# Optimization experiments

Measured on AMD Instinct MI355X. Metric: run time of the kernel, lower is better.

The kernel has to match this reference:

```python
import jax, jax.numpy as jnp
import numpy as np

SIGMA = 10.0
EPSILON = 46.0
BATCH = 4096
D_X = 1024
D_Y = 512


def setup_inputs() -> dict:
    key = jax.random.key(0)
    kx, ky = jax.random.split(key)
    x = jax.random.normal(kx, (BATCH, D_X), dtype=jnp.float32)
    y = jax.random.normal(ky, (BATCH, D_Y), dtype=jnp.float32)
    return {"x": x, "y": y}


def _pairwise_l2(a):
    # [B, B] matrix of ||a_i - a_j||_2 via the matmul trick; safe sqrt for grads.
    sq = jnp.sum(a * a, axis=-1)                      # [B]
    d2 = sq[:, None] + sq[None, :] - 2.0 * (a @ a.T)  # [B, B]
    d2 = jnp.maximum(d2, 0.0)
    return jnp.sqrt(jnp.where(d2 > 1e-12, d2, 1e-12))


def reference(x, y):
    b = x.shape[0]
    dx = _pairwise_l2(x)   # ||x_i - x_j||
    dy = _pairwise_l2(y)   # ||y_i - y_j||
    offdiag = 1.0 - jnp.eye(b, dtype=x.dtype)          # i != j
    mask = offdiag * (dx <= EPSILON).astype(x.dtype)   # threshold at epsilon
    w = jnp.exp(-dx / SIGMA)                           # heat-kernel weight
    loss = jnp.sum(mask * w * dy)
    return loss
```

## Files before the change

### kernel.cpp

```cpp
#include <hip/hip_runtime.h>
#include <hip/hip_bf16.h>
#include <hip/hip_fp8.h>
#include <stdint.h>

#define BATCH 4096
#define D_X   1024
#define D_Y   512

constexpr float SIGMA_INV = 0.1f;
constexpr float EPS_THR   = 46.0f;

constexpr int BMF   = 128;
constexpr int NTF   = BATCH / BMF;
constexpr int NBLKF = NTF * (NTF + 1) / 2;
constexpr int XS8   = D_X / 16;
constexpr int YS8   = D_Y / 16;

constexpr int BM = 128;
constexpr int NT = BATCH / BM;
constexpr int NBLK = NT * (NT + 1) / 2;

typedef __bf16 bf16x8 __attribute__((ext_vector_type(8)));
typedef float  f32x4  __attribute__((ext_vector_type(4)));
typedef unsigned short u16x8 __attribute__((ext_vector_type(8)));
typedef unsigned long long u64;
typedef u64 u64x2 __attribute__((ext_vector_type(2)));

__device__ __forceinline__ unsigned short f32_to_bf16_bits(float f) {
    unsigned int u = __builtin_bit_cast(unsigned int, f);
    unsigned int r = (u + 0x7FFFu + ((u >> 16) & 1u)) >> 16;
    return (unsigned short)r;
}

__device__ __forceinline__ int perm16(int u8) {
    int ks = u8 >> 2, kg = u8 & 3;
    return (ks >> 1) * 8 + kg * 2 + (ks & 1);
}

__global__ void __launch_bounds__(192)
convert_fp8(const float* __restrict__ x, const float* __restrict__ y,
            u64* __restrict__ xq, u64* __restrict__ yq,
            float* __restrict__ sqx, float* __restrict__ sqy) {
    __shared__ float part[2];
    const int row = blockIdx.x;
    const int t   = threadIdx.x;
    const int lane = t & 63;
    const int wid  = t >> 6;

    float nrm = 0.f;
    if (t < 128) {
        const float4* p = (const float4*)(x + (size_t)row * D_X + t * 8);
        float4 f0 = p[0], f1 = p[1];
        float e[8] = {f0.x, f0.y, f0.z, f0.w, f1.x, f1.y, f1.z, f1.w};
        u64 w = 0;
#pragma unroll
        for (int i = 0; i < 8; ++i) {
            __hip_fp8_e4m3 q(e[i]);
            float b = (float)q;
            nrm = fmaf(b, b, nrm);
            w |= (u64)q.__x << (8 * i);
        }
        xq[(size_t)row * 128 + (t & ~15) + perm16(t & 15)] = w;
    } else {
        int o = t - 128;
        const float4* p = (const float4*)(y + (size_t)row * D_Y + o * 8);
        float4 f0 = p[0], f1 = p[1];
        float e[8] = {f0.x, f0.y, f0.z, f0.w, f1.x, f1.y, f1.z, f1.w};
        u64 w = 0;
#pragma unroll
        for (int i = 0; i < 8; ++i) {
            __hip_fp8_e4m3 q(e[i]);
            float b = (float)q;
            nrm = fmaf(b, b, nrm);
            w |= (u64)q.__x << (8 * i);
        }
        yq[(size_t)row * 64 + (o & ~15) + perm16(o & 15)] = w;
    }
#pragma unroll
    for (int off = 32; off > 0; off >>= 1)
        nrm += __shfl_down(nrm, off, 64);
    if (lane == 0) {
        if (wid < 2) part[wid] = nrm;
        else         sqy[row] = nrm;
    }
    __syncthreads();
    if (t == 0) sqx[row] = part[0] + part[1];
}


__device__ __forceinline__ u64x2 ldsfrag2(const u16x8* T, int row, int c) {
    int slot = c ^ (row & 7);
    return __builtin_bit_cast(u64x2, T[row * 8 + slot]);
}

#define ISSUE(DST, BASE, OFF)                                              \
    {                                                                      \
        _Pragma("unroll")                                                  \
        for (int it = 0; it < 8; ++it)                                     \
            __builtin_amdgcn_global_load_lds(                              \
                (const uint32_t __attribute__((address_space(1)))*)(BASE[it] + (OFF)), \
                (uint32_t __attribute__((address_space(3)))*)((DST) + it * 256 + wid * 64), \
                16, 0, 0);                                                 \
    }

#define FRAGS_READ(BUF)                                                    \
        u64x2 fa[2][4], fb[2][4];                      \
        _Pragma("unroll")                                                  \
        for (int t2 = 0; t2 < 2; ++t2) {                                   \
            _Pragma("unroll")                                              \
            for (int m = 0; m < 4; ++m)                                    \
                fa[t2][m] = ldsfrag2(BUF, wr * 64 + m * 16 + lrow,         \
                                     t2 * 4 + kgrp);                       \
            _Pragma("unroll")                                              \
            for (int n = 0; n < 4; ++n)                                    \
                fb[t2][n] = ldsfrag2(BUF, 128 + wc * 64 + n * 16 + lrow,   \
                                     t2 * 4 + kgrp);                       \
        }

#define FRAGS_MFMA(ACC)                                                    \
        __builtin_amdgcn_s_setprio(1);                                     \
        _Pragma("unroll")                                                  \
        for (int t2 = 0; t2 < 2; ++t2)                                     \
            _Pragma("unroll")                                              \
            for (int h = 0; h < 2; ++h)                                    \
                _Pragma("unroll")                                          \
                for (int m = 0; m < 4; ++m)                                \
                    _Pragma("unroll")                                      \
                    for (int n = 0; n < 4; ++n)                            \
                        ACC[m][n] =                                        \
                            __builtin_amdgcn_mfma_f32_16x16x32_fp8_fp8(    \
                                (long)fa[t2][m][h], (long)fb[t2][n][h],    \
                                ACC[m][n], 0, 0, 0);                       \
        __builtin_amdgcn_s_setprio(0);

#define GSTEP(BUF, ACC, W, IBASE, IOFF)                                    \
    {                                                                      \
        asm volatile("s_waitcnt vmcnt(" #W ")" ::: "memory");              \
        __builtin_amdgcn_s_barrier();                                      \
        FRAGS_READ(BUF)                                                    \
        asm volatile("s_waitcnt lgkmcnt(0)" ::: "memory");                 \
        __builtin_amdgcn_s_barrier();                                      \
        ISSUE(BUF, IBASE, IOFF)                                            \
        FRAGS_MFMA(ACC)                                                    \
    }
#define GSTEP_NOISSUE(BUF, ACC, W)                                         \
    {                                                                      \
        asm volatile("s_waitcnt vmcnt(" #W ")" ::: "memory");              \
        __builtin_amdgcn_s_barrier();                                      \
        FRAGS_READ(BUF)                                                    \
        FRAGS_MFMA(ACC)                                                    \
    }

__global__ void __launch_bounds__(256, 2)
gram_fp8(const u16x8* __restrict__ xq, const u16x8* __restrict__ yq,
         const float* __restrict__ sqx, const float* __restrict__ sqy,
         float* __restrict__ out) {
    __shared__ u16x8 T0[2048], T1[2048];
    __shared__ float snxA[BMF], snxB[BMF], snyA[BMF], snyB[BMF];
    __shared__ float wsum[4];

    const int tid  = threadIdx.x;
    const int lane = tid & 63;
    const int wid  = tid >> 6;
    const int wr   = wid >> 1;
    const int wc   = wid & 1;
    const int lrow = lane & 15;
    const int kgrp = lane >> 4;

    int sb = (blockIdx.x & 7) * (NBLKF / 8) + (blockIdx.x >> 3);

    int t0 = sb, bi = 0;
    while (t0 >= NTF - bi) { t0 -= NTF - bi; ++bi; }
    const int bj = bi + t0;
    const int iA = bi * BMF;
    const int iB = bj * BMF;
    const bool diag = (bi == bj);

    if (tid < BMF) {
        snxA[tid] = sqx[iA + tid];
        snyA[tid] = sqy[iA + tid];
    } else {
        int u = tid - BMF;
        snxB[u] = sqx[iB + u];
        snyB[u] = sqy[iB + u];
    }

    const char* g[8];
#pragma unroll
    for (int it = 0; it < 8; ++it) {
        int ul   = it * 256 + wid * 64 + lane;
        int row  = ul >> 3;
        int st   = ul & 7;
        int lg   = st ^ (row & 7);
        int grow = (row < 128 ? iA + row : iB + row - 128);
        g[it] = (const char*)xq + (size_t)grow * (XS8 * 16) + lg * 16;
    }

    f32x4 accX[4][4] = {};
    f32x4 accY[4][4] = {};

    ISSUE(T0, g, 0)
    ISSUE(T1, g, 128)

    GSTEP(T0, accX, 8, g, 256)
    GSTEP(T1, accX, 8, g, 384)
    GSTEP(T0, accX, 8, g, 512)
    GSTEP(T1, accX, 8, g, 640)
    GSTEP(T0, accX, 8, g, 768)
    GSTEP(T1, accX, 8, g, 896)

#pragma unroll
    for (int it = 0; it < 8; ++it) {
        int ul   = it * 256 + wid * 64 + lane;
        int row  = ul >> 3;
        int st   = ul & 7;
        int lg   = st ^ (row & 7);
        int grow = (row < 128 ? iA + row : iB + row - 128);
        g[it] = (const char*)yq + (size_t)grow * (YS8 * 16) + lg * 16;
    }

    GSTEP(T0, accX, 8, g, 0)
    GSTEP(T1, accX, 8, g, 128)
    GSTEP(T0, accY, 8, g, 256)
    GSTEP(T1, accY, 8, g, 384)
    GSTEP_NOISSUE(T0, accY, 8)
    GSTEP_NOISSUE(T1, accY, 0)

    float local = 0.f;
#pragma unroll
    for (int m = 0; m < 4; ++m) {
#pragma unroll
        for (int n = 0; n < 4; ++n) {
            int col   = wc * 64 + n * 16 + lrow;
            float sxj = snxB[col];
            float syj = snyB[col];
#pragma unroll
            for (int r = 0; r < 4; ++r) {
                int rowi  = wr * 64 + m * 16 + kgrp * 4 + r;
                float d2x = snxA[rowi] + sxj - 2.f * accX[m][n][r];
                float dxv = sqrtf(fmaxf(d2x, 1e-12f));
                float d2y = snyA[rowi] + syj - 2.f * accY[m][n][r];
                float dyv = sqrtf(fmaxf(d2y, 1e-12f));
                int gi = iA + rowi, gj = iB + col;
                bool keep = (gi != gj) && (dxv <= EPS_THR);
                float contrib = __expf(-dxv * SIGMA_INV) * dyv;
                local += keep ? contrib : 0.f;
            }
        }
    }
    if (!diag) local *= 2.f;

#pragma unroll
    for (int off = 32; off > 0; off >>= 1)
        local += __shfl_down(local, off, 64);
    if (lane == 0) wsum[wid] = local;
    __syncthreads();
    if (tid == 0)
        atomicAdd(out, wsum[0] + wsum[1] + wsum[2] + wsum[3]);
}

__global__ void norms_kernel_fb(const float* __restrict__ x,
                                const float* __restrict__ y,
                                float* __restrict__ sqx,
                                float* __restrict__ sqy) {
    int row = blockIdx.x;
    int t   = threadIdx.x;
    const float4* xr = (const float4*)(x + (size_t)row * D_X);
    float sx = 0.f;
#pragma unroll
    for (int i = 0; i < D_X / 4 / 64; ++i) {
        float4 v = xr[t + i * 64];
        sx += v.x * v.x + v.y * v.y + v.z * v.z + v.w * v.w;
    }
    const float4* yr = (const float4*)(y + (size_t)row * D_Y);
    float sy = 0.f;
#pragma unroll
    for (int i = 0; i < D_Y / 4 / 64; ++i) {
        float4 v = yr[t + i * 64];
        sy += v.x * v.x + v.y * v.y + v.z * v.z + v.w * v.w;
    }
#pragma unroll
    for (int off = 32; off > 0; off >>= 1) {
        sx += __shfl_down(sx, off, 64);
        sy += __shfl_down(sy, off, 64);
    }
    if (t == 0) { sqx[row] = sx; sqy[row] = sy; }
}

__device__ __forceinline__ void stage_tile_fb(const float* __restrict__ src, int ld,
                                              int base_row, int k0,
                                              u16x8* __restrict__ dst, int tid) {
#pragma unroll
    for (int it = 0; it < 2; ++it) {
        int u   = tid + it * 256;
        int row = u >> 2;
        int q   = u & 3;
        const float4* p = (const float4*)(src + (size_t)(base_row + row) * ld + k0 + q * 16);
        float4 f0 = p[0], f1 = p[1], f2 = p[2], f3 = p[3];
        u16x8 lo, hi;
        lo[0] = f32_to_bf16_bits(f0.x); lo[1] = f32_to_bf16_bits(f0.y);
        lo[2] = f32_to_bf16_bits(f0.z); lo[3] = f32_to_bf16_bits(f0.w);
        lo[4] = f32_to_bf16_bits(f1.x); lo[5] = f32_to_bf16_bits(f1.y);
        lo[6] = f32_to_bf16_bits(f1.z); lo[7] = f32_to_bf16_bits(f1.w);
        hi[0] = f32_to_bf16_bits(f2.x); hi[1] = f32_to_bf16_bits(f2.y);
        hi[2] = f32_to_bf16_bits(f2.z); hi[3] = f32_to_bf16_bits(f2.w);
        hi[4] = f32_to_bf16_bits(f3.x); hi[5] = f32_to_bf16_bits(f3.y);
        hi[6] = f32_to_bf16_bits(f3.z); hi[7] = f32_to_bf16_bits(f3.w);
        int swz = row & 7;
        dst[row * 8 + ((2 * q) ^ swz)]     = lo;
        dst[row * 8 + ((2 * q + 1) ^ swz)] = hi;
    }
}

__device__ __forceinline__ void mfma16_fb(const bf16x8 a[4], const bf16x8 b[4],
                                          f32x4 acc[4][4]) {
#pragma unroll
    for (int m = 0; m < 4; ++m)
#pragma unroll
        for (int n = 0; n < 4; ++n)
            acc[m][n] = __builtin_amdgcn_mfma_f32_16x16x32_bf16(
                a[m], b[n], acc[m][n], 0, 0, 0);
}

__device__ __forceinline__ void load_frags_fb(const u16x8* As_, const u16x8* Bs_,
                                              int wr, int wc, int lrow, int kgrp,
                                              bf16x8 a[2][4], bf16x8 b[2][4]) {
#pragma unroll
    for (int ks = 0; ks < 2; ++ks) {
#pragma unroll
        for (int m = 0; m < 4; ++m) {
            int row  = wr * 64 + m * 16 + lrow;
            int slot = (ks * 4 + kgrp) ^ (row & 7);
            a[ks][m] = __builtin_bit_cast(bf16x8, As_[row * 8 + slot]);
        }
#pragma unroll
        for (int n = 0; n < 4; ++n) {
            int row  = wc * 64 + n * 16 + lrow;
            int slot = (ks * 4 + kgrp) ^ (row & 7);
            b[ks][n] = __builtin_bit_cast(bf16x8, Bs_[row * 8 + slot]);
        }
    }
}

__global__ void __launch_bounds__(256, 2)
graph_loss_fb(const float* __restrict__ x, const float* __restrict__ y,
              const float* __restrict__ sqx, const float* __restrict__ sqy,
              float* __restrict__ out) {
    __shared__ u16x8 As[BM * 8];
    __shared__ u16x8 Bs[BM * 8];
    __shared__ float snxA[BM], snxB[BM], snyA[BM], snyB[BM];
    __shared__ float wsum[4];

    const int tid  = threadIdx.x;
    const int lane = tid & 63;
    const int wid  = tid >> 6;
    const int wr   = wid >> 1;
    const int wc   = wid & 1;
    const int lrow = lane & 15;
    const int kgrp = lane >> 4;

    int t = blockIdx.x, bi = 0;
    while (t >= NT - bi) { t -= NT - bi; ++bi; }
    const int bj = bi + t;
    const int iA = bi * BM;
    const int iB = bj * BM;

    if (tid < BM) {
        snxA[tid] = sqx[iA + tid];
        snyA[tid] = sqy[iA + tid];
        snxB[tid] = sqx[iB + tid];
        snyB[tid] = sqy[iB + tid];
    }

    f32x4 accX[4][4] = {};
    f32x4 accY[4][4] = {};
    bf16x8 a[2][4], b[2][4];

    for (int kt = 0; kt < D_X / 64; ++kt) {
        __syncthreads();
        stage_tile_fb(x, D_X, iA, kt * 64, As, tid);
        stage_tile_fb(x, D_X, iB, kt * 64, Bs, tid);
        __syncthreads();
        load_frags_fb(As, Bs, wr, wc, lrow, kgrp, a, b);
#pragma unroll
        for (int ks = 0; ks < 2; ++ks) mfma16_fb(a[ks], b[ks], accX);
    }
    for (int kt = 0; kt < D_Y / 64; ++kt) {
        __syncthreads();
        stage_tile_fb(y, D_Y, iA, kt * 64, As, tid);
        stage_tile_fb(y, D_Y, iB, kt * 64, Bs, tid);
        __syncthreads();
        load_frags_fb(As, Bs, wr, wc, lrow, kgrp, a, b);
#pragma unroll
        for (int ks = 0; ks < 2; ++ks) mfma16_fb(a[ks], b[ks], accY);
    }

    float local = 0.f;
#pragma unroll
    for (int m = 0; m < 4; ++m) {
#pragma unroll
        for (int n = 0; n < 4; ++n) {
            int col   = wc * 64 + n * 16 + lrow;
            float sxj = snxB[col];
            float syj = snyB[col];
#pragma unroll
            for (int r = 0; r < 4; ++r) {
                int rowi  = wr * 64 + m * 16 + kgrp * 4 + r;
                float d2x = snxA[rowi] + sxj - 2.f * accX[m][n][r];
                float dxv = sqrtf(fmaxf(d2x, 1e-12f));
                float d2y = snyA[rowi] + syj - 2.f * accY[m][n][r];
                float dyv = sqrtf(fmaxf(d2y, 1e-12f));
                int gi = iA + rowi, gj = iB + col;
                bool keep = (gi != gj) && (dxv <= EPS_THR);
                float contrib = __expf(-dxv * SIGMA_INV) * dyv;
                local += keep ? contrib : 0.f;
            }
        }
    }
    if (bi != bj) local *= 2.f;

#pragma unroll
    for (int off = 32; off > 0; off >>= 1)
        local += __shfl_down(local, off, 64);
    if (lane == 0) wsum[wid] = local;
    __syncthreads();
    if (tid == 0)
        atomicAdd(out, wsum[0] + wsum[1] + wsum[2] + wsum[3]);
}

extern "C" void kernel_launch(void* const* d_in, const int* in_sizes, int n_in,
                              void* d_out, int out_size, void* d_ws, size_t ws_size,
                              hipStream_t stream) {
    const float* x = (const float*)d_in[0];
    const float* y = (const float*)d_in[1];
    float* out = (float*)d_out;

    hipMemsetAsync(d_out, 0, sizeof(float) * (size_t)out_size, stream);

    const size_t xq_bytes = (size_t)BATCH * D_X;
    const size_t yq_bytes = (size_t)BATCH * D_Y;
    const size_t sq_bytes = 2 * (size_t)BATCH * sizeof(float);
    const size_t need = xq_bytes + yq_bytes + sq_bytes;

    if (ws_size >= need) {
        u64*   xq  = (u64*)d_ws;
        u64*   yq  = (u64*)((char*)d_ws + xq_bytes);
        float* sqx = (float*)((char*)d_ws + xq_bytes + yq_bytes);
        float* sqy = sqx + BATCH;
        convert_fp8<<<BATCH, 192, 0, stream>>>(x, y, xq, yq, sqx, sqy);
        gram_fp8<<<NBLKF, 256, 0, stream>>>((const u16x8*)xq, (const u16x8*)yq,
                                            sqx, sqy, out);
    } else {
        float* sqx = (float*)d_ws;
        float* sqy = sqx + BATCH;
        norms_kernel_fb<<<BATCH, 64, 0, stream>>>(x, y, sqx, sqy);
        graph_loss_fb<<<NBLK, 256, 0, stream>>>(x, y, sqx, sqy, out);
    }
}
```

Baseline: 57.33 us.

## Halve fp8 gram K-step to 64 bytes, raise occupancy to four blocks per CU

Shrinks each pipelined K-tile from 128 to 64 fp8 bytes per row, halving the LDS double buffers, and raises the launch bound to 4 blocks per SM. The fp8 packing permutation, the LDS layout (pairs of rows share a 128-byte line instead of using an XOR swizzle) and the fragment reads are reworked to match. The aim is more resident waves to hide load latency and fewer fragment registers. The cost is twice as many barrier-synchronised steps and possible LDS bank conflicts without the swizzle.

Result: slower. 59.52 us (+3.8%).

```diff
diff --git a/kernel.cpp b/kernel.cpp
--- a/kernel.cpp
+++ b/kernel.cpp
@@ -13,8 +13,8 @@
 constexpr int BMF   = 128;
 constexpr int NTF   = BATCH / BMF;
 constexpr int NBLKF = NTF * (NTF + 1) / 2;
-constexpr int XS8   = D_X / 16;
-constexpr int YS8   = D_Y / 16;
+constexpr int XRB   = D_X;
+constexpr int YRB   = D_Y;
 
 constexpr int BM = 128;
 constexpr int NT = BATCH / BM;
@@ -32,9 +32,8 @@
     return (unsigned short)r;
 }
 
-__device__ __forceinline__ int perm16(int u8) {
-    int ks = u8 >> 2, kg = u8 & 3;
-    return (ks >> 1) * 8 + kg * 2 + (ks & 1);
+__device__ __forceinline__ int perm8(int ug) {
+    return (ug & 3) * 2 + ((ug >> 2) & 1);
 }
 
 __global__ void __launch_bounds__(192)
@@ -60,7 +59,7 @@
             nrm = fmaf(b, b, nrm);
             w |= (u64)q.__x << (8 * i);
         }
-        xq[(size_t)row * 128 + (t & ~15) + perm16(t & 15)] = w;
+        xq[(size_t)row * 128 + (t & ~7) + perm8(t & 7)] = w;
     } else {
         int o = t - 128;
         const float4* p = (const float4*)(y + (size_t)row * D_Y + o * 8);
@@ -74,7 +73,7 @@
             nrm = fmaf(b, b, nrm);
             w |= (u64)q.__x << (8 * i);
         }
-        yq[(size_t)row * 64 + (o & ~15) + perm16(o & 15)] = w;
+        yq[(size_t)row * 64 + (o & ~7) + perm8(o & 7)] = w;
     }
 #pragma unroll
     for (int off = 32; off > 0; off >>= 1)
@@ -88,15 +87,10 @@
 }
 
 
-__device__ __forceinline__ u64x2 ldsfrag2(const u16x8* T, int row, int c) {
-    int slot = c ^ (row & 7);
-    return __builtin_bit_cast(u64x2, T[row * 8 + slot]);
-}
-
 #define ISSUE(DST, BASE, OFF)                                              \
     {                                                                      \
         _Pragma("unroll")                                                  \
-        for (int it = 0; it < 8; ++it)                                     \
+        for (int it = 0; it < 4; ++it)                                     \
             __builtin_amdgcn_global_load_lds(                              \
                 (const uint32_t __attribute__((address_space(1)))*)(BASE[it] + (OFF)), \
                 (uint32_t __attribute__((address_space(3)))*)((DST) + it * 256 + wid * 64), \
@@ -104,33 +98,30 @@
     }
 
 #define FRAGS_READ(BUF)                                                    \
-        u64x2 fa[2][4], fb[2][4];                      \
+        u64x2 fa[4], fb[4];                                                \
         _Pragma("unroll")                                                  \
-        for (int t2 = 0; t2 < 2; ++t2) {                                   \
-            _Pragma("unroll")                                              \
-            for (int m = 0; m < 4; ++m)                                    \
-                fa[t2][m] = ldsfrag2(BUF, wr * 64 + m * 16 + lrow,         \
-                                     t2 * 4 + kgrp);                       \
-            _Pragma("unroll")                                              \
-            for (int n = 0; n < 4; ++n)                                    \
-                fb[t2][n] = ldsfrag2(BUF, 128 + wc * 64 + n * 16 + lrow,   \
-                                     t2 * 4 + kgrp);                       \
+        for (int m = 0; m < 4; ++m) {                                      \
+            int row = wr * 64 + m * 16 + lrow;                             \
+            fa[m] = __builtin_bit_cast(u64x2,                              \
+                (BUF)[(row >> 1) * 8 + (row & 1) * 4 + kgrp]);             \
+        }                                                                  \
+        _Pragma("unroll")                                                  \
+        for (int n = 0; n < 4; ++n) {                                      \
+            int row = 128 + wc * 64 + n * 16 + lrow;                       \
+            fb[n] = __builtin_bit_cast(u64x2,                              \
+                (BUF)[(row >> 1) * 8 + (row & 1) * 4 + kgrp]);             \
         }
 
 #define FRAGS_MFMA(ACC)                                                    \
         __builtin_amdgcn_s_setprio(1);                                     \
         _Pragma("unroll")                                                  \
-        for (int t2 = 0; t2 < 2; ++t2)                                     \
+        for (int h = 0; h < 2; ++h)                                        \
             _Pragma("unroll")                                              \
-            for (int h = 0; h < 2; ++h)                                    \
+            for (int m = 0; m < 4; ++m)                                    \
                 _Pragma("unroll")                                          \
-                for (int m = 0; m < 4; ++m)                                \
-                    _Pragma("unroll")                                      \
-                    for (int n = 0; n < 4; ++n)                            \
-                        ACC[m][n] =                                        \
-                            __builtin_amdgcn_mfma_f32_16x16x32_fp8_fp8(    \
-                                (long)fa[t2][m][h], (long)fb[t2][n][h],    \
-                                ACC[m][n], 0, 0, 0);                       \
+                for (int n = 0; n < 4; ++n)                                \
+                    ACC[m][n] = __builtin_amdgcn_mfma_f32_16x16x32_fp8_fp8(\
+                        (long)fa[m][h], (long)fb[n][h], ACC[m][n], 0,0,0); \
         __builtin_amdgcn_s_setprio(0);
 
 #define GSTEP(BUF, ACC, W, IBASE, IOFF)                                    \
@@ -151,11 +142,11 @@
         FRAGS_MFMA(ACC)                                                    \
     }
 
-__global__ void __launch_bounds__(256, 2)
+__global__ void __launch_bounds__(256, 4)
 gram_fp8(const u16x8* __restrict__ xq, const u16x8* __restrict__ yq,
          const float* __restrict__ sqx, const float* __restrict__ sqy,
          float* __restrict__ out) {
-    __shared__ u16x8 T0[2048], T1[2048];
+    __shared__ u16x8 T0[1024], T1[1024];
     __shared__ float snxA[BMF], snxB[BMF], snyA[BMF], snyB[BMF];
     __shared__ float wsum[4];
 
@@ -185,45 +176,47 @@
         snyB[u] = sqy[iB + u];
     }
 
-    const char* g[8];
-#pragma unroll
-    for (int it = 0; it < 8; ++it) {
+    const char* gx[4];
+    const char* gy[4];
+#pragma unroll
+    for (int it = 0; it < 4; ++it) {
         int ul   = it * 256 + wid * 64 + lane;
-        int row  = ul >> 3;
-        int st   = ul & 7;
-        int lg   = st ^ (row & 7);
+        int row  = 2 * (ul >> 3) + ((ul >> 2) & 1);
+        int cg   = ul & 3;
         int grow = (row < 128 ? iA + row : iB + row - 128);
-        g[it] = (const char*)xq + (size_t)grow * (XS8 * 16) + lg * 16;
+        gx[it] = (const char*)xq + (size_t)grow * XRB + cg * 16;
+        gy[it] = (const char*)yq + (size_t)grow * YRB + cg * 16;
     }
 
     f32x4 accX[4][4] = {};
     f32x4 accY[4][4] = {};
 
-    ISSUE(T0, g, 0)
-    ISSUE(T1, g, 128)
-
-    GSTEP(T0, accX, 8, g, 256)
-    GSTEP(T1, accX, 8, g, 384)
-    GSTEP(T0, accX, 8, g, 512)
-    GSTEP(T1, accX, 8, g, 640)
-    GSTEP(T0, accX, 8, g, 768)
-    GSTEP(T1, accX, 8, g, 896)
-
-#pragma unroll
-    for (int it = 0; it < 8; ++it) {
-        int ul   = it * 256 + wid * 64 + lane;
-        int row  = ul >> 3;
-        int st   = ul & 7;
-        int lg   = st ^ (row & 7);
-        int grow = (row < 128 ? iA + row : iB + row - 128);
-        g[it] = (const char*)yq + (size_t)grow * (YS8 * 16) + lg * 16;
-    }
-
-    GSTEP(T0, accX, 8, g, 0)
-    GSTEP(T1, accX, 8, g, 128)
-    GSTEP(T0, accY, 8, g, 256)
-    GSTEP(T1, accY, 8, g, 384)
-    GSTEP_NOISSUE(T0, accY, 8)
+    ISSUE(T0, gx, 0)
+    ISSUE(T1, gx, 64)
+
+    GSTEP(T0, accX, 4, gx, 128)
+    GSTEP(T1, accX, 4, gx, 192)
+    GSTEP(T0, accX, 4, gx, 256)
+    GSTEP(T1, accX, 4, gx, 320)
+    GSTEP(T0, accX, 4, gx, 384)
+    GSTEP(T1, accX, 4, gx, 448)
+    GSTEP(T0, accX, 4, gx, 512)
+    GSTEP(T1, accX, 4, gx, 576)
+    GSTEP(T0, accX, 4, gx, 640)
+    GSTEP(T1, accX, 4, gx, 704)
+    GSTEP(T0, accX, 4, gx, 768)
+    GSTEP(T1, accX, 4, gx, 832)
+    GSTEP(T0, accX, 4, gx, 896)
+    GSTEP(T1, accX, 4, gx, 960)
+    GSTEP(T0, accX, 4, gy, 0)
+    GSTEP(T1, accX, 4, gy, 64)
+    GSTEP(T0, accY, 4, gy, 128)
+    GSTEP(T1, accY, 4, gy, 192)
+    GSTEP(T0, accY, 4, gy, 256)
+    GSTEP(T1, accY, 4, gy, 320)
+    GSTEP(T0, accY, 4, gy, 384)
+    GSTEP(T1, accY, 4, gy, 448)
+    GSTEP_NOISSUE(T0, accY, 4)
     GSTEP_NOISSUE(T1, accY, 0)
 
     float local = 0.f;
```
